# Optimization experiments

Hardware: AMD Instinct MI355X
Metric: run time of the kernel (lower is better)

Reference implementation:

```python
import jax, jax.numpy as jnp
import numpy as np

N, F_IN, H, E, G = 100000, 128, 64, 1600000, 256
BN_EPS = 1e-5


def setup_inputs() -> dict:
    key = jax.random.key(0)
    ks = jax.random.split(key, 32)
    rn = lambda k, shp, s=0.1: jax.random.normal(k, shp, jnp.float32) * s
    ru = lambda k, shp: jax.random.uniform(k, shp, jnp.float32)
    inp = {
        'x': jax.random.normal(ks[0], (N, F_IN), jnp.float32),
        'edge_index': jax.random.randint(ks[1], (2, E), 0, N),
        'batch': jnp.sort(jax.random.randint(ks[2], (N,), 0, G)),
        'w0': rn(ks[3], (F_IN, H)), 'b0': rn(ks[4], (H,)),
        'w1': rn(ks[5], (H, H)), 'b1': rn(ks[6], (H,)),
        'w2': rn(ks[7], (H, H)), 'b2': rn(ks[8], (H,)),
        'g0': ru(ks[9], (H,)) + 0.5, 'beta0': rn(ks[10], (H,)),
        'm0': rn(ks[11], (H,)), 'v0': ru(ks[12], (H,)) + 0.5,
        'g1': ru(ks[13], (H,)) + 0.5, 'beta1': rn(ks[14], (H,)),
        'm1': rn(ks[15], (H,)), 'v1': ru(ks[16], (H,)) + 0.5,
        'g2': ru(ks[17], (H,)) + 0.5, 'beta2': rn(ks[18], (H,)),
        'm2': rn(ks[19], (H,)), 'v2': ru(ks[20], (H,)) + 0.5,
        'l1w': rn(ks[21], (H, H // 2)), 'l1b': rn(ks[22], (H // 2,)),
        'l2w': rn(ks[23], (H // 2, 2)), 'l2b': rn(ks[24], (2,)),
    }
    return inp


def reference(x, edge_index, batch, w0, b0, w1, b1, w2, b2,
              g0, beta0, m0, v0, g1, beta1, m1, v1, g2, beta2, m2, v2,
              l1w, l1b, l2w, l2b):
    n = x.shape[0]
    # GCN: add self-loops, symmetric normalization deg^{-1/2} A_hat deg^{-1/2}
    loop = jnp.arange(n)
    src = jnp.concatenate([edge_index[0], loop])
    dst = jnp.concatenate([edge_index[1], loop])
    deg = jax.ops.segment_sum(jnp.ones_like(src, dtype=x.dtype), dst, num_segments=n)
    dinv = jax.lax.rsqrt(jnp.maximum(deg, 1.0))  # deg >= 1 after self-loops
    norm = (dinv[src] * dinv[dst])[:, None]      # [E+N, 1]

    def gcn(h, w, b):
        h = h @ w                                              # [N, H]
        agg = jax.ops.segment_sum(h[src] * norm, dst, num_segments=n)
        return agg + b

    def bn(h, g, be, m, v):  # eval-mode BatchNorm1d (running stats)
        return (h - m) * (g * jax.lax.rsqrt(v + BN_EPS)) + be

    h = jax.nn.relu(bn(gcn(x, w0, b0), g0, beta0, m0, v0))
    h = jax.nn.relu(bn(gcn(h, w1, b1), g1, beta1, m1, v1))
    h = jax.nn.relu(bn(gcn(h, w2, b2), g2, beta2, m2, v2))
    pooled = jax.ops.segment_sum(h, batch, num_segments=G)     # global_add_pool
    h = jax.nn.relu(pooled @ l1w + l1b)
    return h @ l2w + l2b                                        # [G, 2]
```

## Files before the change

kernel.cpp:

```cpp
#include <hip/hip_runtime.h>
#include <hip/hip_bf16.h>

#define BN_EPS 1e-5f

typedef short bf16x8 __attribute__((ext_vector_type(8)));
typedef float f32x4 __attribute__((ext_vector_type(4)));

static __device__ __forceinline__ unsigned short f2bf(float f) {
    unsigned u = __float_as_uint(f);
    unsigned r = (u + 0x7FFF + ((u >> 16) & 1)) >> 16;
    return (unsigned short)r;
}
static __device__ __forceinline__ float bf2f(unsigned short s) {
    return __uint_as_float((unsigned)s << 16);
}
__device__ __forceinline__ int pad4i(int c) { return (c + 3) & ~3; }

#define BIN_SHIFT 9
#define BIN_NODES 512
#define P1_CHUNK 4096
#define P1_THREADS 512
#define IMG_CAP 12288
#define BUILD_THREADS 512

__global__ __launch_bounds__(P1_THREADS) void phase1_kernel(
        const int* __restrict__ src, const int* __restrict__ dst,
        int* __restrict__ bincur, int* __restrict__ ebuf, int e, int ecap) {
    __shared__ int hist[256], base[256], cur[256];
    int t = threadIdx.x;
    int c0 = blockIdx.x * P1_CHUNK;
    if (t < 256) { hist[t] = 0; }
    __syncthreads();
    bool full = (c0 + P1_CHUNK <= e) &&
                (((((unsigned long long)(const void*)dst) |
                   ((unsigned long long)(const void*)src)) & 15ull) == 0ull);
    if (full) {
        const int4* d4 = (const int4*)(dst + c0);
        int4 da = d4[t], db = d4[t + P1_THREADS];
        atomicAdd(&hist[da.x >> BIN_SHIFT], 1);
        atomicAdd(&hist[da.y >> BIN_SHIFT], 1);
        atomicAdd(&hist[da.z >> BIN_SHIFT], 1);
        atomicAdd(&hist[da.w >> BIN_SHIFT], 1);
        atomicAdd(&hist[db.x >> BIN_SHIFT], 1);
        atomicAdd(&hist[db.y >> BIN_SHIFT], 1);
        atomicAdd(&hist[db.z >> BIN_SHIFT], 1);
        atomicAdd(&hist[db.w >> BIN_SHIFT], 1);
        __syncthreads();
        if (t < 256) {
            if (hist[t] > 0)
                base[t] = t * ecap + atomicAdd(&bincur[t], hist[t]);
            cur[t] = 0;
        }
        __syncthreads();
        const int4* s4 = (const int4*)(src + c0);
        int4 sa = s4[t], sb = s4[t + P1_THREADS];
#define P1_SCAT(D, S)                                                         \
        {                                                                     \
            int b_ = (D) >> BIN_SHIFT;                                        \
            int r_ = atomicAdd(&cur[b_], 1);                                  \
            int p_ = base[b_] + r_;                                           \
            if (p_ < (b_ + 1) * ecap)                                         \
                ebuf[p_] = (S) | (((D) & (BIN_NODES - 1)) << 17);             \
        }
        P1_SCAT(da.x, sa.x) P1_SCAT(da.y, sa.y) P1_SCAT(da.z, sa.z) P1_SCAT(da.w, sa.w)
        P1_SCAT(db.x, sb.x) P1_SCAT(db.y, sb.y) P1_SCAT(db.z, sb.z) P1_SCAT(db.w, sb.w)
    } else {
        int iend = c0 + P1_CHUNK; if (iend > e) iend = e;
        int dreg[8];
#pragma unroll
        for (int u = 0; u < 8; u++) {
            int i = c0 + t + u * P1_THREADS;
            if (i < iend) {
                int d = dst[i];
                dreg[u] = d;
                atomicAdd(&hist[d >> BIN_SHIFT], 1);
            }
        }
        __syncthreads();
        if (t < 256) {
            if (hist[t] > 0)
                base[t] = t * ecap + atomicAdd(&bincur[t], hist[t]);
            cur[t] = 0;
        }
        __syncthreads();
#pragma unroll
        for (int u = 0; u < 8; u++) {
            int i = c0 + t + u * P1_THREADS;
            if (i < iend) {
                int s = src[i], d = dreg[u];
                P1_SCAT(d, s)
            }
        }
#undef P1_SCAT
    }
}

__global__ __launch_bounds__(BUILD_THREADS) void build_kernel(
        const int* __restrict__ ebuf, const int* __restrict__ bincur, int ecap,
        float* __restrict__ dinv, int* __restrict__ row_start,
        int* __restrict__ row_len, int* __restrict__ gtotal,
        int* __restrict__ csr, int* __restrict__ gcursor,
        unsigned short* __restrict__ ha_sent, int n, int sentinel) {
    __shared__ int image[IMG_CAP];
    __shared__ int c512[BIN_NODES];
    __shared__ int sd[BIN_NODES];
    __shared__ int rl[BIN_NODES];
    __shared__ int lcur[BIN_NODES];
    __shared__ int rbs;
    int b = blockIdx.x, t = threadIdx.x;
    if (b == 0 && t < 64) ha_sent[t] = 0;
    c512[t] = 0;
    lcur[t] = 0;
    __syncthreads();
    int cnt_b = bincur[b]; if (cnt_b > ecap) cnt_b = ecap;
    int e0 = b * ecap;
    int cnt4 = cnt_b >> 2, rem = cnt_b & 3;
    const int4* eb4 = (const int4*)(ebuf + e0);
    for (int j = t; j < cnt4; j += BUILD_THREADS) {
        int4 v = eb4[j];
        atomicAdd(&c512[v.x >> 17], 1);
        atomicAdd(&c512[v.y >> 17], 1);
        atomicAdd(&c512[v.z >> 17], 1);
        atomicAdd(&c512[v.w >> 17], 1);
    }
    if (t < rem) atomicAdd(&c512[ebuf[e0 + cnt4 * 4 + t] >> 17], 1);
    __syncthreads();
    int n0 = b * BIN_NODES;
    int deg = c512[t];
    if (n0 + t < n) dinv[n0 + t] = rsqrtf((float)(deg + 1));
    int pv = pad4i(deg);
    sd[t] = pv;
    __syncthreads();
    for (int off = 1; off < BIN_NODES; off <<= 1) {
        int x = (t >= off) ? sd[t - off] : 0;
        __syncthreads();
        sd[t] += x;
        __syncthreads();
    }
    int excl = sd[t] - pv;
    rl[t] = excl;
    if (t == BIN_NODES - 1) rbs = atomicAdd(gtotal, sd[BIN_NODES - 1]);
    __syncthreads();
    int rb = rbs;
    int rspan = sd[BIN_NODES - 1];
    if (n0 + t < n) {
        row_start[n0 + t] = rb + excl;
        row_len[n0 + t] = pv;
    }
    if (rspan <= IMG_CAP) {
        for (int k = t; k < rspan; k += BUILD_THREADS) image[k] = sentinel;
        __syncthreads();
        for (int j = t; j < cnt4; j += BUILD_THREADS) {
            int4 v = eb4[j];
#define B_SCAT(EN)                                                            \
            {                                                                 \
                int dl_ = (EN) >> 17;                                         \
                int pos_ = rl[dl_] + atomicAdd(&lcur[dl_], 1);                \
                image[pos_] = (EN) & 0x1FFFF;                                 \
            }
            B_SCAT(v.x) B_SCAT(v.y) B_SCAT(v.z) B_SCAT(v.w)
        }
        if (t < rem) { int en = ebuf[e0 + cnt4 * 4 + t]; B_SCAT(en) }
        __syncthreads();
        for (int k = t; k < rspan; k += BUILD_THREADS) csr[rb + k] = image[k];
    } else {
        int nloc = n - n0; if (nloc > BIN_NODES) nloc = BIN_NODES;
        if (t < nloc) gcursor[n0 + t] = 0;
        __syncthreads();
        for (int j = t; j < cnt_b; j += BUILD_THREADS) {
            int en = ebuf[e0 + j];
            int s = en & 0x1FFFF;
            int dl = en >> 17;
            int pos = rb + rl[dl] + atomicAdd(&gcursor[n0 + dl], 1);
            csr[pos] = s;
        }
        __syncthreads();
        if (t < nloc) {
            int st = rb + rl[t] + gcursor[n0 + t];
            int en2 = rb + rl[t] + pv;
            for (int pos = st; pos < en2; pos++) csr[pos] = sentinel;
        }
#undef B_SCAT
    }
}

template<int K, bool BF16IN>
__global__ __launch_bounds__(256) void lin_mfma(const void* __restrict__ in_,
                                                const float* __restrict__ w,
                                                const float* __restrict__ dinv,
                                                unsigned short* __restrict__ outbf, int n) {
    constexpr int XS = K + 8;
    __shared__ unsigned short xs[64 * XS];
    __shared__ unsigned short wt[64 * XS];
    int t = threadIdx.x;
    int row0 = blockIdx.x * 64;
    int nrows = n - row0; if (nrows > 64) nrows = 64;

    {
        const float4* w4 = (const float4*)w;
        for (int idx = t; idx < K * 16; idx += 256) {
            int k = idx >> 4, c4 = (idx & 15) * 4;
            float4 v = w4[idx];
            wt[(c4 + 0) * XS + k] = f2bf(v.x);
            wt[(c4 + 1) * XS + k] = f2bf(v.y);
            wt[(c4 + 2) * XS + k] = f2bf(v.z);
            wt[(c4 + 3) * XS + k] = f2bf(v.w);
        }
    }
    if constexpr (BF16IN) {
        const uint4* in4 = (const uint4*)((const unsigned short*)in_ + (size_t)row0 * K);
        int total8 = nrows * (K / 8);
        for (int idx = t; idx < total8; idx += 256) {
            int r = idx / (K / 8), kk = idx - r * (K / 8);
            uint4 v = in4[idx];
            *(uint4*)&xs[r * XS + kk * 8] = v;
        }
    } else {
        const float4* in4 = (const float4*)((const float*)in_ + (size_t)row0 * K);
        int total4 = nrows * (K / 4);
        for (int idx = t; idx < total4; idx += 256) {
            int r = idx / (K / 4), kk = idx - r * (K / 4);
            float4 v = in4[idx];
            ushort4 s4;
            s4.x = f2bf(v.x); s4.y = f2bf(v.y); s4.z = f2bf(v.z); s4.w = f2bf(v.w);
            *(ushort4*)&xs[r * XS + kk * 4] = s4;
        }
    }
    __syncthreads();

    int lane = t & 63;
    int wid = t >> 6;
    int quad = lane >> 4;
    int l15 = lane & 15;

    f32x4 acc[4];
#pragma unroll
    for (int cg_ = 0; cg_ < 4; cg_++) acc[cg_] = (f32x4){0.f, 0.f, 0.f, 0.f};

    const unsigned short* xrow = &xs[(wid * 16 + l15) * XS + quad * 8];
#pragma unroll
    for (int kc = 0; kc < K / 32; kc++) {
        bf16x8 bfrag = *(const bf16x8*)(xrow + kc * 32);
#pragma unroll
        for (int cg_ = 0; cg_ < 4; cg_++) {
            bf16x8 afrag = *(const bf16x8*)&wt[(cg_ * 16 + l15) * XS + kc * 32 + quad * 8];
            acc[cg_] = __builtin_amdgcn_mfma_f32_16x16x32_bf16(afrag, bfrag, acc[cg_], 0, 0, 0);
        }
    }

    int grow = row0 + wid * 16 + l15;
    if (grow < n) {
        float dv = dinv[grow];
#pragma unroll
        for (int cg_ = 0; cg_ < 4; cg_++) {
            ushort4 st;
            st.x = f2bf(acc[cg_][0] * dv);
            st.y = f2bf(acc[cg_][1] * dv);
            st.z = f2bf(acc[cg_][2] * dv);
            st.w = f2bf(acc[cg_][3] * dv);
            *(ushort4*)&outbf[(size_t)grow * 64 + cg_ * 16 + quad * 4] = st;
        }
    }
}

template<bool POOL>
__global__ __launch_bounds__(256) void agg_kernel(
        const unsigned short* __restrict__ hs, const int* __restrict__ row_start,
        const int* __restrict__ row_len, const int* __restrict__ csr,
        const float* __restrict__ dinv,
        const float* __restrict__ bias, const float* __restrict__ gam,
        const float* __restrict__ bet, const float* __restrict__ mu,
        const float* __restrict__ var,
        unsigned short* __restrict__ out,
        const int* __restrict__ batch, float* __restrict__ pooled, int n) {
    int iw = blockIdx.x * 4 + (threadIdx.x >> 6);
    unsigned lane = threadIdx.x & 63;
    if (iw >= n) return;
    int i = __builtin_amdgcn_readfirstlane(iw);
    float acc = bf2f(hs[((unsigned)i << 6) + lane]);
    int rs = __builtin_amdgcn_readfirstlane(row_start[i]);
    int re = rs + __builtin_amdgcn_readfirstlane(row_len[i]);
    int j = rs;
    for (; j + 16 <= re; j += 16) {
        int s0 = __builtin_amdgcn_readfirstlane(csr[j + 0]);
        int s1 = __builtin_amdgcn_readfirstlane(csr[j + 1]);
        int s2 = __builtin_amdgcn_readfirstlane(csr[j + 2]);
        int s3 = __builtin_amdgcn_readfirstlane(csr[j + 3]);
        int s4 = __builtin_amdgcn_readfirstlane(csr[j + 4]);
        int s5 = __builtin_amdgcn_readfirstlane(csr[j + 5]);
        int s6 = __builtin_amdgcn_readfirstlane(csr[j + 6]);
        int s7 = __builtin_amdgcn_readfirstlane(csr[j + 7]);
        int s8 = __builtin_amdgcn_readfirstlane(csr[j + 8]);
        int s9 = __builtin_amdgcn_readfirstlane(csr[j + 9]);
        int sA = __builtin_amdgcn_readfirstlane(csr[j + 10]);
        int sB = __builtin_amdgcn_readfirstlane(csr[j + 11]);
        int sC = __builtin_amdgcn_readfirstlane(csr[j + 12]);
        int sD = __builtin_amdgcn_readfirstlane(csr[j + 13]);
        int sE = __builtin_amdgcn_readfirstlane(csr[j + 14]);
        int sF = __builtin_amdgcn_readfirstlane(csr[j + 15]);
        float h0 = bf2f(hs[((unsigned)s0 << 6) + lane]);
        float h1 = bf2f(hs[((unsigned)s1 << 6) + lane]);
        float h2 = bf2f(hs[((unsigned)s2 << 6) + lane]);
        float h3 = bf2f(hs[((unsigned)s3 << 6) + lane]);
        float h4 = bf2f(hs[((unsigned)s4 << 6) + lane]);
        float h5 = bf2f(hs[((unsigned)s5 << 6) + lane]);
        float h6 = bf2f(hs[((unsigned)s6 << 6) + lane]);
        float h7 = bf2f(hs[((unsigned)s7 << 6) + lane]);
        float h8 = bf2f(hs[((unsigned)s8 << 6) + lane]);
        float h9 = bf2f(hs[((unsigned)s9 << 6) + lane]);
        float hA = bf2f(hs[((unsigned)sA << 6) + lane]);
        float hB = bf2f(hs[((unsigned)sB << 6) + lane]);
        float hC = bf2f(hs[((unsigned)sC << 6) + lane]);
        float hD = bf2f(hs[((unsigned)sD << 6) + lane]);
        float hE = bf2f(hs[((unsigned)sE << 6) + lane]);
        float hF = bf2f(hs[((unsigned)sF << 6) + lane]);
        acc += (((h0 + h1) + (h2 + h3)) + ((h4 + h5) + (h6 + h7)))
             + (((h8 + h9) + (hA + hB)) + ((hC + hD) + (hE + hF)));
    }
    for (; j < re; j += 4) {
        int s0 = __builtin_amdgcn_readfirstlane(csr[j + 0]);
        int s1 = __builtin_amdgcn_readfirstlane(csr[j + 1]);
        int s2 = __builtin_amdgcn_readfirstlane(csr[j + 2]);
        int s3 = __builtin_amdgcn_readfirstlane(csr[j + 3]);
        float h0 = bf2f(hs[((unsigned)s0 << 6) + lane]);
        float h1 = bf2f(hs[((unsigned)s1 << 6) + lane]);
        float h2 = bf2f(hs[((unsigned)s2 << 6) + lane]);
        float h3 = bf2f(hs[((unsigned)s3 << 6) + lane]);
        acc += (h0 + h1) + (h2 + h3);
    }
    float agg = acc * dinv[i];
    float scale = gam[lane] * rsqrtf(var[lane] + BN_EPS);
    float r = (agg + bias[lane] - mu[lane]) * scale + bet[lane];
    unsigned short sv = f2bf(r > 0.f ? r : 0.f);
    out[((unsigned)i << 6) + lane] = sv;
    if (POOL) {
        int g = __builtin_amdgcn_readfirstlane(batch[i]);
        atomicAdd(&pooled[(size_t)g * 64 + lane], bf2f(sv));
    }
}

__global__ void mlp_kernel(const float* __restrict__ pooled,
                           const float* __restrict__ l1w, const float* __restrict__ l1b,
                           const float* __restrict__ l2w, const float* __restrict__ l2b,
                           float* __restrict__ out) {
    int g = blockIdx.x;
    int lane = threadIdx.x;
    __shared__ float p[64];
    __shared__ float h1[32];
    p[lane] = pooled[(size_t)g * 64 + lane];
    __syncthreads();
    if (lane < 32) {
        float a = l1b[lane];
#pragma unroll 8
        for (int k = 0; k < 64; k++) a += p[k] * l1w[k * 32 + lane];
        h1[lane] = a > 0.f ? a : 0.f;
    }
    __syncthreads();
    if (lane < 2) {
        float a = l2b[lane];
#pragma unroll 8
        for (int j = 0; j < 32; j++) a += h1[j] * l2w[j * 2 + lane];
        out[g * 2 + lane] = a;
    }
}

extern "C" void kernel_launch(void* const* d_in, const int* in_sizes, int n_in,
                              void* d_out, int out_size, void* d_ws, size_t ws_size,
                              hipStream_t stream) {
    const float* x     = (const float*)d_in[0];
    const int*   ei    = (const int*)d_in[1];
    const int*   batch = (const int*)d_in[2];
    const float* w0 = (const float*)d_in[3];
    const float* b0 = (const float*)d_in[4];
    const float* w1 = (const float*)d_in[5];
    const float* b1 = (const float*)d_in[6];
    const float* w2 = (const float*)d_in[7];
    const float* b2 = (const float*)d_in[8];
    const float* g0 = (const float*)d_in[9];
    const float* be0 = (const float*)d_in[10];
    const float* m0 = (const float*)d_in[11];
    const float* v0 = (const float*)d_in[12];
    const float* g1 = (const float*)d_in[13];
    const float* be1 = (const float*)d_in[14];
    const float* m1 = (const float*)d_in[15];
    const float* v1 = (const float*)d_in[16];
    const float* g2 = (const float*)d_in[17];
    const float* be2 = (const float*)d_in[18];
    const float* m2 = (const float*)d_in[19];
    const float* v2 = (const float*)d_in[20];
    const float* l1w = (const float*)d_in[21];
    const float* l1b = (const float*)d_in[22];
    const float* l2w = (const float*)d_in[23];
    const float* l2b = (const float*)d_in[24];
    float* out = (float*)d_out;

    const int N = in_sizes[2];
    const int E = in_sizes[1] / 2;
    const int G = out_size / 2;
    const int NBINS = (N + BIN_NODES - 1) / BIN_NODES;
    int ECAP = ((2 * (E / NBINS)) + 1023) & ~1023;
    if (ECAP < 2048) ECAP = 2048;

    const int* src = ei;
    const int* dst = ei + E;

    char* p = (char*)d_ws;
    auto alloc = [&](size_t bytes) -> void* {
        void* r = (void*)p;
        p += (bytes + 255) & ~(size_t)255;
        return r;
    };
    const size_t CSR_CAP = (size_t)E + 4 * (size_t)N + 64;
    float* dinvp    = (float*)alloc((size_t)N * 4);
    int*   row_start= (int*)alloc((size_t)N * 4);
    int*   row_len  = (int*)alloc((size_t)N * 4);
    int*   gcursor  = (int*)alloc((size_t)N * 4);
    int*   bincur   = (int*)alloc((size_t)NBINS * 4);
    int*   gtotal   = (int*)alloc(4);
    float* pooled   = (float*)alloc((size_t)G * 64 * 4);
    char*  zero_end = p;
    int*   ebuf     = (int*)alloc((size_t)NBINS * ECAP * 4);
    int*   csr      = (int*)alloc(CSR_CAP * 4);
    unsigned short* h_a = (unsigned short*)alloc((size_t)(N + 1) * 64 * 2);
    unsigned short* h_b = (unsigned short*)alloc((size_t)N * 64 * 2);
    (void)ws_size;

    hipMemsetAsync(bincur, 0, (size_t)(zero_end - (char*)bincur), stream);
    const int nchunks = (E + P1_CHUNK - 1) / P1_CHUNK;
    phase1_kernel<<<nchunks, P1_THREADS, 0, stream>>>(src, dst, bincur, ebuf, E, ECAP);
    build_kernel<<<NBINS, BUILD_THREADS, 0, stream>>>(ebuf, bincur, ECAP, dinvp,
                                                      row_start, row_len, gtotal,
                                                      csr, gcursor,
                                                      h_a + (size_t)N * 64, N, N);

    const int nblk = (N + 3) / 4;
    const int lblk = (N + 63) / 64;
    lin_mfma<128, false><<<lblk, 256, 0, stream>>>(x, w0, dinvp, h_a, N);
    agg_kernel<false><<<nblk, 256, 0, stream>>>(h_a, row_start, row_len, csr, dinvp,
                                                b0, g0, be0, m0, v0, h_b,
                                                batch, pooled, N);
    lin_mfma<64, true><<<lblk, 256, 0, stream>>>(h_b, w1, dinvp, h_a, N);
    agg_kernel<false><<<nblk, 256, 0, stream>>>(h_a, row_start, row_len, csr, dinvp,
                                                b1, g1, be1, m1, v1, h_b,
                                                batch, pooled, N);
    lin_mfma<64, true><<<lblk, 256, 0, stream>>>(h_b, w2, dinvp, h_a, N);
    agg_kernel<true><<<nblk, 256, 0, stream>>>(h_a, row_start, row_len, csr, dinvp,
                                               b2, g2, be2, m2, v2, h_b,
                                               batch, pooled, N);
    mlp_kernel<<<G, 64, 0, stream>>>(pooled, l1w, l1b, l2w, l2b, out);
}
```

Baseline: 350.3 us.

## Split feature tables into lo/hi halves and aggregate two nodes per wave

Stores node feature tables as two 32-column bf16 halves. Alternating blocks each aggregate one half, so the gathered working set per pass shrinks and is more likely to stay cache-resident. Each wave now handles two destination nodes, 32 lanes each, iterating to the longer row and padding the shorter one with sentinel loads. The aim is better L2/MALL locality for the random gathers, at the cost of divergent loop lengths, wasted sentinel loads and per-lane address selection in place of scalar addressing.

```diff
diff --git a/kernel.cpp b/kernel.cpp
--- a/kernel.cpp
+++ b/kernel.cpp
@@ -100,7 +100,8 @@
         float* __restrict__ dinv, int* __restrict__ row_start,
         int* __restrict__ row_len, int* __restrict__ gtotal,
         int* __restrict__ csr, int* __restrict__ gcursor,
-        unsigned short* __restrict__ ha_sent, int n, int sentinel) {
+        unsigned short* __restrict__ sent_lo, unsigned short* __restrict__ sent_hi,
+        int n, int sentinel) {
     __shared__ int image[IMG_CAP];
     __shared__ int c512[BIN_NODES];
     __shared__ int sd[BIN_NODES];
@@ -108,7 +109,7 @@
     __shared__ int lcur[BIN_NODES];
     __shared__ int rbs;
     int b = blockIdx.x, t = threadIdx.x;
-    if (b == 0 && t < 64) ha_sent[t] = 0;
+    if (b == 0 && t < 32) { sent_lo[t] = 0; sent_hi[t] = 0; }
     c512[t] = 0;
     lcur[t] = 0;
     __syncthreads();
@@ -186,9 +187,11 @@
 
 template<int K, bool BF16IN>
 __global__ __launch_bounds__(256) void lin_mfma(const void* __restrict__ in_,
+                                                const unsigned short* __restrict__ in_hi,
                                                 const float* __restrict__ w,
                                                 const float* __restrict__ dinv,
-                                                unsigned short* __restrict__ outbf, int n) {
+                                                unsigned short* __restrict__ out_lo,
+                                                unsigned short* __restrict__ out_hi, int n) {
     constexpr int XS = K + 8;
     __shared__ unsigned short xs[64 * XS];
     __shared__ unsigned short wt[64 * XS];
@@ -208,11 +211,12 @@
         }
     }
     if constexpr (BF16IN) {
-        const uint4* in4 = (const uint4*)((const unsigned short*)in_ + (size_t)row0 * K);
-        int total8 = nrows * (K / 8);
+        const uint4* lo4 = (const uint4*)((const unsigned short*)in_ + (size_t)row0 * 32);
+        const uint4* hi4 = (const uint4*)(in_hi + (size_t)row0 * 32);
+        int total8 = nrows * 8;
         for (int idx = t; idx < total8; idx += 256) {
-            int r = idx / (K / 8), kk = idx - r * (K / 8);
-            uint4 v = in4[idx];
+            int r = idx >> 3, kk = idx & 7;
+            uint4 v = (kk < 4) ? lo4[r * 4 + kk] : hi4[r * 4 + (kk - 4)];
             *(uint4*)&xs[r * XS + kk * 8] = v;
         }
     } else {
@@ -258,88 +262,88 @@
             st.y = f2bf(acc[cg_][1] * dv);
             st.z = f2bf(acc[cg_][2] * dv);
             st.w = f2bf(acc[cg_][3] * dv);
-            *(ushort4*)&outbf[(size_t)grow * 64 + cg_ * 16 + quad * 4] = st;
-        }
-    }
-}
+            if (cg_ < 2)
+                *(ushort4*)&out_lo[(size_t)grow * 32 + cg_ * 16 + quad * 4] = st;
+            else
+                *(ushort4*)&out_hi[(size_t)grow * 32 + (cg_ - 2) * 16 + quad * 4] = st;
+        }
+    }
+}
+
+#define PSLOT(O, H)                                                           \
+    {                                                                         \
+        int sa_ = ((O) < lenA) ? csr[jA + (O)] : sent;                        \
+        int sb_ = ((O) < lenB) ? csr[jB + (O)] : sent;                        \
+        int r_ = nodeB ? sb_ : sa_;                                           \
+        H = bf2f(tbl[((unsigned)r_ << 5) + sub]);                             \
+    }
 
 template<bool POOL>
 __global__ __launch_bounds__(256) void agg_kernel(
-        const unsigned short* __restrict__ hs, const int* __restrict__ row_start,
-        const int* __restrict__ row_len, const int* __restrict__ csr,
-        const float* __restrict__ dinv,
+        const unsigned short* __restrict__ tlo, const unsigned short* __restrict__ thi,
+        const int* __restrict__ row_start, const int* __restrict__ row_len,
+        const int* __restrict__ csr, const float* __restrict__ dinv,
         const float* __restrict__ bias, const float* __restrict__ gam,
         const float* __restrict__ bet, const float* __restrict__ mu,
         const float* __restrict__ var,
-        unsigned short* __restrict__ out,
-        const int* __restrict__ batch, float* __restrict__ pooled, int n) {
-    int iw = blockIdx.x * 4 + (threadIdx.x >> 6);
-    unsigned lane = threadIdx.x & 63;
-    if (iw >= n) return;
-    int i = __builtin_amdgcn_readfirstlane(iw);
-    float acc = bf2f(hs[((unsigned)i << 6) + lane]);
-    int rs = __builtin_amdgcn_readfirstlane(row_start[i]);
-    int re = rs + __builtin_amdgcn_readfirstlane(row_len[i]);
-    int j = rs;
-    for (; j + 16 <= re; j += 16) {
-        int s0 = __builtin_amdgcn_readfirstlane(csr[j + 0]);
-        int s1 = __builtin_amdgcn_readfirstlane(csr[j + 1]);
-        int s2 = __builtin_amdgcn_readfirstlane(csr[j + 2]);
-        int s3 = __builtin_amdgcn_readfirstlane(csr[j + 3]);
-        int s4 = __builtin_amdgcn_readfirstlane(csr[j + 4]);
-        int s5 = __builtin_amdgcn_readfirstlane(csr[j + 5]);
-        int s6 = __builtin_amdgcn_readfirstlane(csr[j + 6]);
-        int s7 = __builtin_amdgcn_readfirstlane(csr[j + 7]);
-        int s8 = __builtin_amdgcn_readfirstlane(csr[j + 8]);
-        int s9 = __builtin_amdgcn_readfirstlane(csr[j + 9]);
-        int sA = __builtin_amdgcn_readfirstlane(csr[j + 10]);
-        int sB = __builtin_amdgcn_readfirstlane(csr[j + 11]);
-        int sC = __builtin_amdgcn_readfirstlane(csr[j + 12]);
-        int sD = __builtin_amdgcn_readfirstlane(csr[j + 13]);
-        int sE = __builtin_amdgcn_readfirstlane(csr[j + 14]);
-        int sF = __builtin_amdgcn_readfirstlane(csr[j + 15]);
-        float h0 = bf2f(hs[((unsigned)s0 << 6) + lane]);
-        float h1 = bf2f(hs[((unsigned)s1 << 6) + lane]);
-        float h2 = bf2f(hs[((unsigned)s2 << 6) + lane]);
-        float h3 = bf2f(hs[((unsigned)s3 << 6) + lane]);
-        float h4 = bf2f(hs[((unsigned)s4 << 6) + lane]);
-        float h5 = bf2f(hs[((unsigned)s5 << 6) + lane]);
-        float h6 = bf2f(hs[((unsigned)s6 << 6) + lane]);
-        float h7 = bf2f(hs[((unsigned)s7 << 6) + lane]);
-        float h8 = bf2f(hs[((unsigned)s8 << 6) + lane]);
-        float h9 = bf2f(hs[((unsigned)s9 << 6) + lane]);
-        float hA = bf2f(hs[((unsigned)sA << 6) + lane]);
-        float hB = bf2f(hs[((unsigned)sB << 6) + lane]);
-        float hC = bf2f(hs[((unsigned)sC << 6) + lane]);
-        float hD = bf2f(hs[((unsigned)sD << 6) + lane]);
-        float hE = bf2f(hs[((unsigned)sE << 6) + lane]);
-        float hF = bf2f(hs[((unsigned)sF << 6) + lane]);
+        unsigned short* __restrict__ olo, unsigned short* __restrict__ ohi,
+        const int* __restrict__ batch,
+        float* __restrict__ plo, float* __restrict__ phi, int n) {
+    int hf = blockIdx.x & 1;
+    int pairIdx = (blockIdx.x >> 1) * 4 + (threadIdx.x >> 6);
+    int lane = threadIdx.x & 63;
+    int iA = pairIdx * 2;
+    if (iA >= n) return;
+    iA = __builtin_amdgcn_readfirstlane(iA);
+    int iB = iA + 1;
+    bool hasB = iB < n;
+    int sent = n;
+    int iBt = hasB ? iB : sent;
+    const unsigned short* tbl = hf ? thi : tlo;
+    unsigned short* otb = hf ? ohi : olo;
+    int sub = lane & 31;
+    int nodeB = lane >> 5;
+    int selfRow = nodeB ? iBt : iA;
+    float acc = bf2f(tbl[((unsigned)selfRow << 5) + sub]);
+    int jA = __builtin_amdgcn_readfirstlane(row_start[iA]);
+    int lenA = __builtin_amdgcn_readfirstlane(row_len[iA]);
+    int jB = hasB ? __builtin_amdgcn_readfirstlane(row_start[iB]) : jA;
+    int lenB = hasB ? __builtin_amdgcn_readfirstlane(row_len[iB]) : 0;
+    int Lmax = lenA > lenB ? lenA : lenB;
+    int k = 0;
+    for (; k + 16 <= Lmax; k += 16) {
+        float h0, h1, h2, h3, h4, h5, h6, h7, h8, h9, hA, hB, hC, hD, hE, hF;
+        PSLOT(k + 0, h0)  PSLOT(k + 1, h1)  PSLOT(k + 2, h2)  PSLOT(k + 3, h3)
+        PSLOT(k + 4, h4)  PSLOT(k + 5, h5)  PSLOT(k + 6, h6)  PSLOT(k + 7, h7)
+        PSLOT(k + 8, h8)  PSLOT(k + 9, h9)  PSLOT(k + 10, hA) PSLOT(k + 11, hB)
+        PSLOT(k + 12, hC) PSLOT(k + 13, hD) PSLOT(k + 14, hE) PSLOT(k + 15, hF)
         acc += (((h0 + h1) + (h2 + h3)) + ((h4 + h5) + (h6 + h7)))
              + (((h8 + h9) + (hA + hB)) + ((hC + hD) + (hE + hF)));
     }
-    for (; j < re; j += 4) {
-        int s0 = __builtin_amdgcn_readfirstlane(csr[j + 0]);
-        int s1 = __builtin_amdgcn_readfirstlane(csr[j + 1]);
-        int s2 = __builtin_amdgcn_readfirstlane(csr[j + 2]);
-        int s3 = __builtin_amdgcn_readfirstlane(csr[j + 3]);
-        float h0 = bf2f(hs[((unsigned)s0 << 6) + lane]);
-        float h1 = bf2f(hs[((unsigned)s1 << 6) + lane]);
-        float h2 = bf2f(hs[((unsigned)s2 << 6) + lane]);
-        float h3 = bf2f(hs[((unsigned)s3 << 6) + lane]);
+    for (; k < Lmax; k += 4) {
+        float h0, h1, h2, h3;
+        PSLOT(k + 0, h0) PSLOT(k + 1, h1) PSLOT(k + 2, h2) PSLOT(k + 3, h3)
         acc += (h0 + h1) + (h2 + h3);
     }
-    float agg = acc * dinv[i];
-    float scale = gam[lane] * rsqrtf(var[lane] + BN_EPS);
-    float r = (agg + bias[lane] - mu[lane]) * scale + bet[lane];
+    int io = nodeB ? iB : iA;
+    bool live = !nodeB || hasB;
+    int fi = hf * 32 + sub;
+    float dv = dinv[live ? io : iA];
+    float scale = gam[fi] * rsqrtf(var[fi] + BN_EPS);
+    float r = (acc * dv + bias[fi] - mu[fi]) * scale + bet[fi];
     unsigned short sv = f2bf(r > 0.f ? r : 0.f);
-    out[((unsigned)i << 6) + lane] = sv;
-    if (POOL) {
-        int g = __builtin_amdgcn_readfirstlane(batch[i]);
-        atomicAdd(&pooled[(size_t)g * 64 + lane], bf2f(sv));
-    }
-}
-
-__global__ void mlp_kernel(const float* __restrict__ pooled,
+    if (live) {
+        otb[((unsigned)io << 5) + sub] = sv;
+        if (POOL) {
+            int g = batch[io];
+            float* pt = hf ? phi : plo;
+            atomicAdd(&pt[(size_t)g * 32 + sub], bf2f(sv));
+        }
+    }
+}
+#undef PSLOT
+
+__global__ void mlp_kernel(const float* __restrict__ plo, const float* __restrict__ phi,
                            const float* __restrict__ l1w, const float* __restrict__ l1b,
                            const float* __restrict__ l2w, const float* __restrict__ l2b,
                            float* __restrict__ out) {
@@ -347,7 +351,8 @@
     int lane = threadIdx.x;
     __shared__ float p[64];
     __shared__ float h1[32];
-    p[lane] = pooled[(size_t)g * 64 + lane];
+    p[lane] = (lane < 32) ? plo[(size_t)g * 32 + lane]
+                          : phi[(size_t)g * 32 + (lane - 32)];
     __syncthreads();
     if (lane < 32) {
         float a = l1b[lane];
@@ -417,12 +422,15 @@
     int*   gcursor  = (int*)alloc((size_t)N * 4);
     int*   bincur   = (int*)alloc((size_t)NBINS * 4);
     int*   gtotal   = (int*)alloc(4);
-    float* pooled   = (float*)alloc((size_t)G * 64 * 4);
+    float* plo      = (float*)alloc((size_t)G * 32 * 4);
+    float* phi      = (float*)alloc((size_t)G * 32 * 4);
     char*  zero_end = p;
     int*   ebuf     = (int*)alloc((size_t)NBINS * ECAP * 4);
     int*   csr      = (int*)alloc(CSR_CAP * 4);
-    unsigned short* h_a = (unsigned short*)alloc((size_t)(N + 1) * 64 * 2);
-    unsigned short* h_b = (unsigned short*)alloc((size_t)N * 64 * 2);
+    unsigned short* ha_lo = (unsigned short*)alloc((size_t)(N + 1) * 32 * 2);
+    unsigned short* ha_hi = (unsigned short*)alloc((size_t)(N + 1) * 32 * 2);
+    unsigned short* hb_lo = (unsigned short*)alloc((size_t)N * 32 * 2);
+    unsigned short* hb_hi = (unsigned short*)alloc((size_t)N * 32 * 2);
     (void)ws_size;
 
     hipMemsetAsync(bincur, 0, (size_t)(zero_end - (char*)bincur), stream);
@@ -431,21 +439,26 @@
     build_kernel<<<NBINS, BUILD_THREADS, 0, stream>>>(ebuf, bincur, ECAP, dinvp,
                                                       row_start, row_len, gtotal,
                                                       csr, gcursor,
-                                                      h_a + (size_t)N * 64, N, N);
-
-    const int nblk = (N + 3) / 4;
+                                                      ha_lo + (size_t)N * 32,
+                                                      ha_hi + (size_t)N * 32, N, N);
+
+    const int pairs = (N + 1) / 2;
+    const int ablk = 2 * ((pairs + 3) / 4);
     const int lblk = (N + 63) / 64;
-    lin_mfma<128, false><<<lblk, 256, 0, stream>>>(x, w0, dinvp, h_a, N);
-    agg_kernel<false><<<nblk, 256, 0, stream>>>(h_a, row_start, row_len, csr, dinvp,
-                                                b0, g0, be0, m0, v0, h_b,
-                                                batch, pooled, N);
-    lin_mfma<64, true><<<lblk, 256, 0, stream>>>(h_b, w1, dinvp, h_a, N);
-    agg_kernel<false><<<nblk, 256, 0, stream>>>(h_a, row_start, row_len, csr, dinvp,
-                                                b1, g1, be1, m1, v1, h_b,
-                                                batch, pooled, N);
-    lin_mfma<64, true><<<lblk, 256, 0, stream>>>(h_b, w2, dinvp, h_a, N);
-    agg_kernel<true><<<nblk, 256, 0, stream>>>(h_a, row_start, row_len, csr, dinvp,
-                                               b2, g2, be2, m2, v2, h_b,
-                                               batch, pooled, N);
-    mlp_kernel<<<G, 64, 0, stream>>>(pooled, l1w, l1b, l2w, l2b, out);
-}
+    lin_mfma<128, false><<<lblk, 256, 0, stream>>>(x, nullptr, w0, dinvp,
+                                                   ha_lo, ha_hi, N);
+    agg_kernel<false><<<ablk, 256, 0, stream>>>(ha_lo, ha_hi, row_start, row_len,
+                                                csr, dinvp, b0, g0, be0, m0, v0,
+                                                hb_lo, hb_hi, batch, plo, phi, N);
+    lin_mfma<64, true><<<lblk, 256, 0, stream>>>(hb_lo, hb_hi, w1, dinvp,
+                                                 ha_lo, ha_hi, N);
+    agg_kernel<false><<<ablk, 256, 0, stream>>>(ha_lo, ha_hi, row_start, row_len,
+                                                csr, dinvp, b1, g1, be1, m1, v1,
+                                                hb_lo, hb_hi, batch, plo, phi, N);
+    lin_mfma<64, true><<<lblk, 256, 0, stream>>>(hb_lo, hb_hi, w2, dinvp,
+                                                 ha_lo, ha_hi, N);
+    agg_kernel<true><<<ablk, 256, 0, stream>>>(ha_lo, ha_hi, row_start, row_len,
+                                               csr, dinvp, b2, g2, be2, m2, v2,
+                                               hb_lo, hb_hi, batch, plo, phi, N);
+    mlp_kernel<<<G, 64, 0, stream>>>(plo, phi, l1w, l1b, l2w, l2b, out);
+}
```

After: 592.4 us. 69.1% more time.
